# Kernel optimization log

Hardware: AMD Instinct MI355X
Metric: run time of the kernel (lower is better)

The kernel has to match this reference:

```python
import jax, jax.numpy as jnp
import numpy as np

N_NODES = 50000
N_EDGES = 800000
D_IN = 128
D_HID = 128
D_OUT = 2


def setup_inputs() -> dict:
    key = jax.random.key(0)
    ks = jax.random.split(key, 8)
    x = jax.random.normal(ks[0], (N_NODES, D_IN), dtype=jnp.float32)
    edge_index = jax.random.randint(ks[1], (2, N_EDGES), 0, N_NODES, dtype=jnp.int64)
    s = 0.05
    W1_l = jax.random.normal(ks[2], (D_HID, D_IN), dtype=jnp.float32) * s
    W1_r = jax.random.normal(ks[3], (D_HID, D_IN), dtype=jnp.float32) * s
    b1 = jax.random.normal(ks[4], (D_HID,), dtype=jnp.float32) * s
    W2_l = jax.random.normal(ks[5], (D_OUT, D_HID), dtype=jnp.float32) * s
    W2_r = jax.random.normal(ks[6], (D_OUT, D_HID), dtype=jnp.float32) * s
    b2 = jax.random.normal(ks[7], (D_OUT,), dtype=jnp.float32) * s
    return {"x": x, "edge_index": edge_index, "W1_l": W1_l, "W1_r": W1_r,
            "b1": b1, "W2_l": W2_l, "W2_r": W2_r, "b2": b2}


def _sage_conv(x, src, dst, W_l, W_r, b):
    # mean-aggregate neighbor features: gather from src, scatter-sum to dst
    n = x.shape[0]
    msg = x[src]                                            # [E, d]
    agg = jax.ops.segment_sum(msg, dst, num_segments=n)      # [n, d]
    cnt = jax.ops.segment_sum(jnp.ones((src.shape[0],), x.dtype), dst,
                              num_segments=n)
    agg = agg / jnp.maximum(cnt, 1.0)[:, None]
    # lin_l(aggregated) + lin_r(self) + bias  (PyG SAGEConv with root_weight)
    return agg @ W_l.T + x @ W_r.T + b


def reference(x, edge_index, W1_l, W1_r, b1, W2_l, W2_r, b2):
    src, dst = edge_index[0], edge_index[1]
    h = _sage_conv(x, src, dst, W1_l, W1_r, b1)
    h = jax.nn.relu(h)
    out = _sage_conv(h, src, dst, W2_l, W2_r, b2)
    return out
```

## Files before the change

### kernel.cpp

```cpp
#include <hip/hip_runtime.h>

#define N_NODES 50000
#define N_EDGES 800000
#define CAP 64

typedef __bf16 bf16_8 __attribute__((ext_vector_type(8)));
typedef float  f32_4  __attribute__((ext_vector_type(4)));


__global__ void prep_kernel(const float* __restrict__ W1l, const float* __restrict__ W1r,
                            __bf16* __restrict__ Wt, const float* __restrict__ x,
                            __bf16* __restrict__ xb, const int* __restrict__ src,
                            const int* __restrict__ dst,
                            int* __restrict__ deg_p, int* __restrict__ bins) {
    int b = blockIdx.x;
    if (b < 3125) {
        int t = b * 256 + threadIdx.x;
        int d = dst[t], s = src[t];
        int pos = atomicAdd(&deg_p[d * 16], 1);
        int node = t >> 4, c8 = t & 15;
        const float4* xp = (const float4*)(x + node * 128 + c8 * 8);
        float4 v0 = xp[0], v1 = xp[1];
        bf16_8 o;
        o[0] = (__bf16)v0.x; o[1] = (__bf16)v0.y; o[2] = (__bf16)v0.z; o[3] = (__bf16)v0.w;
        o[4] = (__bf16)v1.x; o[5] = (__bf16)v1.y; o[6] = (__bf16)v1.z; o[7] = (__bf16)v1.w;
        *(bf16_8*)(xb + t * 8) = o;
        if (pos < CAP) bins[d * CAP + pos] = s;
    } else {
        int t = (b - 3125) * 256 + threadIdx.x;
        int n = t >> 8, k = t & 255;
        float v = (k < 128) ? W1l[n * 128 + k] : W1r[n * 128 + (k - 128)];
        Wt[t] = (__bf16)v;
    }
}

#define LDA 264
__global__ __launch_bounds__(256) void gather_gemm_kernel(
    const int* __restrict__ deg_p, const int* __restrict__ bins,
    const __bf16* __restrict__ xb, const __bf16* __restrict__ Wt,
    const float* __restrict__ b1, const float* __restrict__ W2l,
    const float* __restrict__ W2r, float* __restrict__ y, float* __restrict__ z)
{
    __shared__ __bf16 As[16 * LDA];
    __shared__ float4 sp[4][16];

    const int i0 = blockIdx.x * 16;
    const int tid = threadIdx.x;
    const int row = tid >> 4, c8 = tid & 15;
    const int gi = i0 + row;

    bf16_8 sv = *(const bf16_8*)(xb + gi * 128 + c8 * 8);
    *(bf16_8*)(&As[row * LDA + 128 + c8 * 8]) = sv;

    {
        const int* bp = bins + gi * CAP;
        int n = min(deg_p[gi * 16], CAP);
        float acc[8] = {};
        int j = 0;
        for (; j + 8 <= n; j += 8) {
            int idx[8];
            #pragma unroll
            for (int u = 0; u < 8; ++u) idx[u] = bp[j + u];
            bf16_8 vv[8];
            #pragma unroll
            for (int u = 0; u < 8; ++u)
                vv[u] = *(const bf16_8*)(xb + idx[u] * 128 + c8 * 8);
            #pragma unroll
            for (int u = 0; u < 8; ++u) {
                float s01 = (float)vv[0][u] + (float)vv[1][u];
                float s23 = (float)vv[2][u] + (float)vv[3][u];
                float s45 = (float)vv[4][u] + (float)vv[5][u];
                float s67 = (float)vv[6][u] + (float)vv[7][u];
                acc[u] += (s01 + s23) + (s45 + s67);
            }
        }
        for (; j + 2 <= n; j += 2) {
            int s0 = bp[j], s1 = bp[j + 1];
            bf16_8 v0 = *(const bf16_8*)(xb + s0 * 128 + c8 * 8);
            bf16_8 v1 = *(const bf16_8*)(xb + s1 * 128 + c8 * 8);
            #pragma unroll
            for (int u = 0; u < 8; ++u) acc[u] += (float)v0[u] + (float)v1[u];
        }
        if (j < n) {
            int s0 = bp[j];
            bf16_8 v0 = *(const bf16_8*)(xb + s0 * 128 + c8 * 8);
            #pragma unroll
            for (int u = 0; u < 8; ++u) acc[u] += (float)v0[u];
        }
        float inv = 1.0f / fmaxf((float)n, 1.0f);
        bf16_8 o;
        #pragma unroll
        for (int u = 0; u < 8; ++u) o[u] = (__bf16)(acc[u] * inv);
        *(bf16_8*)(&As[row * LDA + c8 * 8]) = o;
    }
    __syncthreads();

    const int wv = tid >> 6, lane = tid & 63;
    const int mr = lane & 15, q = lane >> 4;
    const int n0 = wv * 2, n1 = wv * 2 + 1;

    f32_4 acc0 = (f32_4){0.f,0.f,0.f,0.f}, acc1 = (f32_4){0.f,0.f,0.f,0.f};
    #pragma unroll
    for (int ks = 0; ks < 8; ++ks) {
        bf16_8 a  = *(const bf16_8*)(&As[mr * LDA + ks * 32 + q * 8]);
        bf16_8 b0 = *(const bf16_8*)(Wt + (n0 * 16 + mr) * 256 + ks * 32 + q * 8);
        bf16_8 bb = *(const bf16_8*)(Wt + (n1 * 16 + mr) * 256 + ks * 32 + q * 8);
        acc0 = __builtin_amdgcn_mfma_f32_16x16x32_bf16(a, b0, acc0, 0, 0, 0);
        acc1 = __builtin_amdgcn_mfma_f32_16x16x32_bf16(a, bb, acc1, 0, 0, 0);
    }

    float py0[4] = {}, py1[4] = {}, pz0[4] = {}, pz1[4] = {};
    #pragma unroll
    for (int ntl = 0; ntl < 2; ++ntl) {
        int col = (wv * 2 + ntl) * 16 + mr;
        f32_4 a = ntl ? acc1 : acc0;
        float bb  = b1[col];
        float wl0 = W2l[col], wl1 = W2l[128 + col];
        float wr0 = W2r[col], wr1 = W2r[128 + col];
        #pragma unroll
        for (int r = 0; r < 4; ++r) {
            float hv = fmaxf(a[r] + bb, 0.f);
            py0[r] += hv * wl0; py1[r] += hv * wl1;
            pz0[r] += hv * wr0; pz1[r] += hv * wr1;
        }
    }
    #pragma unroll
    for (int off = 1; off < 16; off <<= 1) {
        #pragma unroll
        for (int r = 0; r < 4; ++r) {
            py0[r] += __shfl_xor(py0[r], off);
            py1[r] += __shfl_xor(py1[r], off);
            pz0[r] += __shfl_xor(pz0[r], off);
            pz1[r] += __shfl_xor(pz1[r], off);
        }
    }
    if (mr < 4) {
        int r = mr;
        sp[wv][q * 4 + r] = make_float4(py0[r], py1[r], pz0[r], pz1[r]);
    }
    __syncthreads();

    if (tid < 16) {
        float4 a0 = sp[0][tid], a1 = sp[1][tid], a2 = sp[2][tid], a3 = sp[3][tid];
        ((float2*)y)[i0 + tid] = make_float2(a0.x + a1.x + a2.x + a3.x,
                                             a0.y + a1.y + a2.y + a3.y);
        ((float2*)z)[i0 + tid] = make_float2(a0.z + a1.z + a2.z + a3.z,
                                             a0.w + a1.w + a2.w + a3.w);
    }
}

__global__ void final_kernel(const int* __restrict__ deg_p, const int* __restrict__ bins,
                             const float* __restrict__ y, const float* __restrict__ z,
                             const float* __restrict__ b2, float* __restrict__ out) {
    int t = blockIdx.x * 256 + threadIdx.x;
    int node = t >> 3, p = t & 7;
    if (node >= N_NODES) return;
    const int* bp = bins + node * CAP;
    int n = min(deg_p[node * 16], CAP);
    float a0 = 0.f, a1 = 0.f;
    for (int j = p; j < n; j += 8) {
        float2 v = ((const float2*)y)[bp[j]];
        a0 += v.x; a1 += v.y;
    }
    a0 += __shfl_xor(a0, 1); a1 += __shfl_xor(a1, 1);
    a0 += __shfl_xor(a0, 2); a1 += __shfl_xor(a1, 2);
    a0 += __shfl_xor(a0, 4); a1 += __shfl_xor(a1, 4);
    if (p == 0) {
        float inv = 1.0f / fmaxf((float)n, 1.0f);
        float2 zz = ((const float2*)z)[node];
        ((float2*)out)[node] = make_float2(a0 * inv + zz.x + b2[0],
                                           a1 * inv + zz.y + b2[1]);
    }
}

extern "C" void kernel_launch(void* const* d_in, const int* in_sizes, int n_in,
                              void* d_out, int out_size, void* d_ws, size_t ws_size,
                              hipStream_t stream) {
    const float* x   = (const float*)d_in[0];
    const int*   ei  = (const int*)  d_in[1];
    const float* W1l = (const float*)d_in[2];
    const float* W1r = (const float*)d_in[3];
    const float* b1  = (const float*)d_in[4];
    const float* W2l = (const float*)d_in[5];
    const float* W2r = (const float*)d_in[6];
    const float* b2  = (const float*)d_in[7];
    float* out = (float*)d_out;
    const int* src = ei;
    const int* dst = ei + N_EDGES;

    char* ws = (char*)d_ws;
    int*    deg_p = (int*)   (ws + 0);
    int*    bins  = (int*)   (ws + 3200000);
    __bf16* xb    = (__bf16*)(ws + 16000000);
    float*  y     = (float*) (ws + 28800000);
    float*  z     = (float*) (ws + 29200000);
    __bf16* Wt    = (__bf16*)(ws + 29600000);

    hipMemsetAsync(deg_p, 0, 3200000, stream);
    prep_kernel<<<3253, 256, 0, stream>>>(W1l, W1r, Wt, x, xb, src, dst, deg_p, bins);
    gather_gemm_kernel<<<3125, 256, 0, stream>>>(deg_p, bins, xb, Wt, b1, W2l, W2r, y, z);
    final_kernel<<<1563, 256, 0, stream>>>(deg_p, bins, y, z, b2, out);
}
```

Before: 183.3 us.

## Store neighbor bins as 16-bit indices and rebalance prep and final kernels

```diff
diff --git a/kernel.cpp b/kernel.cpp
--- a/kernel.cpp
+++ b/kernel.cpp
@@ -6,28 +6,46 @@
 
 typedef __bf16 bf16_8 __attribute__((ext_vector_type(8)));
 typedef float  f32_4  __attribute__((ext_vector_type(4)));
+typedef unsigned short u16;
 
 
 __global__ void prep_kernel(const float* __restrict__ W1l, const float* __restrict__ W1r,
                             __bf16* __restrict__ Wt, const float* __restrict__ x,
                             __bf16* __restrict__ xb, const int* __restrict__ src,
                             const int* __restrict__ dst,
-                            int* __restrict__ deg_p, int* __restrict__ bins) {
+                            int* __restrict__ deg_p, u16* __restrict__ bins) {
     int b = blockIdx.x;
-    if (b < 3125) {
+    if (b < 1563) {
         int t = b * 256 + threadIdx.x;
-        int d = dst[t], s = src[t];
-        int pos = atomicAdd(&deg_p[d * 16], 1);
-        int node = t >> 4, c8 = t & 15;
-        const float4* xp = (const float4*)(x + node * 128 + c8 * 8);
-        float4 v0 = xp[0], v1 = xp[1];
-        bf16_8 o;
-        o[0] = (__bf16)v0.x; o[1] = (__bf16)v0.y; o[2] = (__bf16)v0.z; o[3] = (__bf16)v0.w;
-        o[4] = (__bf16)v1.x; o[5] = (__bf16)v1.y; o[6] = (__bf16)v1.z; o[7] = (__bf16)v1.w;
-        *(bf16_8*)(xb + t * 8) = o;
-        if (pos < CAP) bins[d * CAP + pos] = s;
+        if (t < 400000) {
+            int d0 = dst[t],          s0 = src[t];
+            int d1 = dst[t + 400000], s1 = src[t + 400000];
+            int p0 = atomicAdd(&deg_p[d0 * 16], 1);
+            int p1 = atomicAdd(&deg_p[d1 * 16], 1);
+            {
+                int node = t >> 4, c8 = t & 15;
+                const float4* xp = (const float4*)(x + node * 128 + c8 * 8);
+                float4 v0 = xp[0], v1 = xp[1];
+                bf16_8 o;
+                o[0] = (__bf16)v0.x; o[1] = (__bf16)v0.y; o[2] = (__bf16)v0.z; o[3] = (__bf16)v0.w;
+                o[4] = (__bf16)v1.x; o[5] = (__bf16)v1.y; o[6] = (__bf16)v1.z; o[7] = (__bf16)v1.w;
+                *(bf16_8*)(xb + t * 8) = o;
+            }
+            {
+                int t2 = t + 400000;
+                int node = t2 >> 4, c8 = t2 & 15;
+                const float4* xp = (const float4*)(x + node * 128 + c8 * 8);
+                float4 v0 = xp[0], v1 = xp[1];
+                bf16_8 o;
+                o[0] = (__bf16)v0.x; o[1] = (__bf16)v0.y; o[2] = (__bf16)v0.z; o[3] = (__bf16)v0.w;
+                o[4] = (__bf16)v1.x; o[5] = (__bf16)v1.y; o[6] = (__bf16)v1.z; o[7] = (__bf16)v1.w;
+                *(bf16_8*)(xb + t2 * 8) = o;
+            }
+            if (p0 < CAP) bins[d0 * CAP + p0] = (u16)s0;
+            if (p1 < CAP) bins[d1 * CAP + p1] = (u16)s1;
+        }
     } else {
-        int t = (b - 3125) * 256 + threadIdx.x;
+        int t = (b - 1563) * 256 + threadIdx.x;
         int n = t >> 8, k = t & 255;
         float v = (k < 128) ? W1l[n * 128 + k] : W1r[n * 128 + (k - 128)];
         Wt[t] = (__bf16)v;
@@ -36,7 +54,7 @@
 
 #define LDA 264
 __global__ __launch_bounds__(256) void gather_gemm_kernel(
-    const int* __restrict__ deg_p, const int* __restrict__ bins,
+    const int* __restrict__ deg_p, const u16* __restrict__ bins,
     const __bf16* __restrict__ xb, const __bf16* __restrict__ Wt,
     const float* __restrict__ b1, const float* __restrict__ W2l,
     const float* __restrict__ W2r, float* __restrict__ y, float* __restrict__ z)
@@ -53,7 +71,7 @@
     *(bf16_8*)(&As[row * LDA + 128 + c8 * 8]) = sv;
 
     {
-        const int* bp = bins + gi * CAP;
+        const u16* bp = bins + gi * CAP;
         int n = min(deg_p[gi * 16], CAP);
         float acc[8] = {};
         int j = 0;
@@ -149,22 +167,22 @@
     }
 }
 
-__global__ void final_kernel(const int* __restrict__ deg_p, const int* __restrict__ bins,
+__global__ void final_kernel(const int* __restrict__ deg_p, const u16* __restrict__ bins,
                              const float* __restrict__ y, const float* __restrict__ z,
                              const float* __restrict__ b2, float* __restrict__ out) {
     int t = blockIdx.x * 256 + threadIdx.x;
-    int node = t >> 3, p = t & 7;
-    if (node >= N_NODES) return;
-    const int* bp = bins + node * CAP;
+    int node = t >> 4, p = t & 15;
+    const u16* bp = bins + node * CAP;
     int n = min(deg_p[node * 16], CAP);
     float a0 = 0.f, a1 = 0.f;
-    for (int j = p; j < n; j += 8) {
+    for (int j = p; j < n; j += 16) {
         float2 v = ((const float2*)y)[bp[j]];
         a0 += v.x; a1 += v.y;
     }
     a0 += __shfl_xor(a0, 1); a1 += __shfl_xor(a1, 1);
     a0 += __shfl_xor(a0, 2); a1 += __shfl_xor(a1, 2);
     a0 += __shfl_xor(a0, 4); a1 += __shfl_xor(a1, 4);
+    a0 += __shfl_xor(a0, 8); a1 += __shfl_xor(a1, 8);
     if (p == 0) {
         float inv = 1.0f / fmaxf((float)n, 1.0f);
         float2 zz = ((const float2*)z)[node];
@@ -190,14 +208,14 @@
 
     char* ws = (char*)d_ws;
     int*    deg_p = (int*)   (ws + 0);
-    int*    bins  = (int*)   (ws + 3200000);
-    __bf16* xb    = (__bf16*)(ws + 16000000);
-    float*  y     = (float*) (ws + 28800000);
-    float*  z     = (float*) (ws + 29200000);
-    __bf16* Wt    = (__bf16*)(ws + 29600000);
+    u16*    bins  = (u16*)   (ws + 3200000);
+    __bf16* xb    = (__bf16*)(ws + 9600000);
+    float*  y     = (float*) (ws + 22400000);
+    float*  z     = (float*) (ws + 22800000);
+    __bf16* Wt    = (__bf16*)(ws + 23200000);
 
     hipMemsetAsync(deg_p, 0, 3200000, stream);
-    prep_kernel<<<3253, 256, 0, stream>>>(W1l, W1r, Wt, x, xb, src, dst, deg_p, bins);
+    prep_kernel<<<1691, 256, 0, stream>>>(W1l, W1r, Wt, x, xb, src, dst, deg_p, bins);
     gather_gemm_kernel<<<3125, 256, 0, stream>>>(deg_p, bins, xb, Wt, b1, W2l, W2r, y, z);
-    final_kernel<<<1563, 256, 0, stream>>>(deg_p, bins, y, z, b2, out);
-}
+    final_kernel<<<3125, 256, 0, stream>>>(deg_p, bins, y, z, b2, out);
+}
```

New measurement: 184.7 us. No clear change (+0.7%).
